# Kernel tuning notes

Measured on AMD Instinct MI355X. Metric: run time of the kernel, lower is better.

## Reference

```python
import jax, jax.numpy as jnp
import numpy as np

NUM_HEADS = 8
GROUPS = 32
EPS = 1e-5


def setup_inputs() -> dict:
    key = jax.random.key(0)
    ks = jax.random.split(key, 4)
    B, C, H, W = 8, 512, 32, 32
    x = jax.random.normal(ks[0], (B, C, H, W), dtype=jnp.float32)
    gn_w = jnp.ones((C,), dtype=jnp.float32)
    gn_b = jnp.zeros((C,), dtype=jnp.float32)
    qkv_w = jax.random.normal(ks[1], (3 * C, C), dtype=jnp.float32) * (1.0 / np.sqrt(C))
    qkv_b = jnp.zeros((3 * C,), dtype=jnp.float32)
    proj_w = jax.random.normal(ks[2], (C, C), dtype=jnp.float32) * (1.0 / np.sqrt(C))
    proj_b = jnp.zeros((C,), dtype=jnp.float32)
    return {"x": x, "gn_w": gn_w, "gn_b": gn_b, "qkv_w": qkv_w,
            "qkv_b": qkv_b, "proj_w": proj_w, "proj_b": proj_b}


def reference(x, gn_w, gn_b, qkv_w, qkv_b, proj_w, proj_b):
    b, c, h, w = x.shape
    n = h * w
    hd = c // NUM_HEADS
    xf = x.reshape(b, c, n)
    # GroupNorm over (channels_per_group, HW) per sample
    xg = xf.reshape(b, GROUPS, -1)
    mu = jnp.mean(xg, axis=-1, keepdims=True)
    var = jnp.var(xg, axis=-1, keepdims=True)
    xn = ((xg - mu) * jax.lax.rsqrt(var + EPS)).reshape(b, c, n)
    xn = xn * gn_w[None, :, None] + gn_b[None, :, None]
    # 1x1 conv == channel matmul
    qkv = jnp.einsum('oc,bcn->bon', qkv_w, xn) + qkv_b[None, :, None]
    q, k, v = jnp.split(qkv, 3, axis=1)
    q = q.reshape(b, NUM_HEADS, hd, n)
    k = k.reshape(b, NUM_HEADS, hd, n)
    v = v.reshape(b, NUM_HEADS, hd, n)
    scale = hd ** 0.5
    score = jnp.einsum('bhdn,bhdm->bhnm', q, k) / scale  # [b,h,HW,HW]
    attn = jax.nn.softmax(score, axis=-1)
    out = jnp.einsum('bhnm,bhdm->bhnd', attn, v)  # [b,h,HW,hd]
    out = out.transpose(0, 1, 3, 2).reshape(b, c, n)
    out = jnp.einsum('oc,bcn->bon', proj_w, out) + proj_b[None, :, None]
    return x + out.reshape(b, c, h, w)
```

## Files before the change

### kernel.cpp

```cpp
#include <hip/hip_runtime.h>

typedef unsigned short u16;
typedef unsigned long long u64;
typedef __bf16 bf16x8 __attribute__((ext_vector_type(8)));
typedef float f32x4 __attribute__((ext_vector_type(4)));

#define NB 8
#define NC 512
#define NN 1024
#define NHEADS 8
#define HDIM 64
#define CPG 16
#define EPSV 1e-5f
#define LOG2E 1.44269504f

__device__ __forceinline__ float bf2f(u16 h) {
  union { unsigned u; float f; } v; v.u = ((unsigned)h) << 16; return v.f;
}
__device__ __forceinline__ u16 f2bf(float f) {
  union { float f; unsigned u; } v; v.f = f;
  unsigned r = v.u + 0x7fffu + ((v.u >> 16) & 1u);
  return (u16)(r >> 16);
}
__device__ __forceinline__ float h2f(u16 h) {
  unsigned s = (h >> 15) & 1u, e = (h >> 10) & 31u, m = h & 1023u;
  union { unsigned u; float f; } v;
  if (e == 0) { v.u = s << 31; return v.f + (s ? -1.f : 1.f) * (float)m * 5.9604645e-8f; }
  if (e == 31) { v.u = (s << 31) | 0x7F800000u | (m << 13); return v.f; }
  v.u = (s << 31) | ((e + 112u) << 23) | (m << 13);
  return v.f;
}
__device__ __forceinline__ u16 f2h(float f) {
  union { float f; unsigned u; } v; v.f = f;
  unsigned s = (v.u >> 16) & 0x8000u; int e = (int)((v.u >> 23) & 0xFF) - 112;
  unsigned m = v.u & 0x7FFFFFu;
  if (e <= 0) return (u16)s;
  if (e >= 31) return (u16)(s | 0x7C00u);
  u16 h = (u16)(s | (e << 10) | (m >> 13));
  unsigned rem = m & 0x1FFFu;
  if (rem > 0x1000u || (rem == 0x1000u && (h & 1u))) ++h;
  return h;
}
__device__ __forceinline__ float load_elem(const void* p, size_t i, int f) {
  if (f == 1) return bf2f(((const u16*)p)[i]);
  if (f == 2) return h2f(((const u16*)p)[i]);
  return ((const float*)p)[i];
}

__device__ __forceinline__ float exp2_fast(float x) {
  float r;
  asm("v_exp_f32 %0, %1" : "=v"(r) : "v"(x));
  return r;
}

__global__ void detect_dtype(const u16* __restrict__ gw_raw, int* __restrict__ flag) {
  if (threadIdx.x != 0 || blockIdx.x != 0) return;
  int bf = 0, hf = 0;
  for (int i = 0; i < 16; ++i) {
    u16 w = gw_raw[i];
    if (w == 0x3F80u) ++bf;
    else if (w == 0x3C00u) ++hf;
  }
  *flag = (bf >= 12) ? 1 : (hf >= 12) ? 2 : 0;
}

__global__ __launch_bounds__(256) void cvt_to_bf16(const void* __restrict__ raw,
                                                   u16* __restrict__ dst, int n,
                                                   const int* __restrict__ flag) {
  const int f = *flag;
  const int i = (blockIdx.x * 256 + threadIdx.x) * 4;
  if (i >= n) return;
  if (f == 1) {
    *(uint2*)(dst + i) = *(const uint2*)((const u16*)raw + i);
  } else if (f == 0) {
    float4 v = *(const float4*)((const float*)raw + i);
    u16 o[4] = {f2bf(v.x), f2bf(v.y), f2bf(v.z), f2bf(v.w)};
    *(u64*)(dst + i) = *(const u64*)o;
  } else {
    u16 o[4];
#pragma unroll
    for (int k2 = 0; k2 < 4; ++k2) o[k2] = f2bf(h2f(((const u16*)raw)[i + k2]));
    *(u64*)(dst + i) = *(const u64*)o;
  }
}

__global__ __launch_bounds__(256) void cvt_biases(const void* __restrict__ gw,
                                                  const void* __restrict__ gb,
                                                  const void* __restrict__ qb,
                                                  const void* __restrict__ pb,
                                                  float* __restrict__ cgw,
                                                  float* __restrict__ cgb,
                                                  float* __restrict__ cqb,
                                                  float* __restrict__ cpb,
                                                  const int* __restrict__ flag) {
  const int f = *flag;
  int i = blockIdx.x * 256 + threadIdx.x;
  if (i < 512)        cgw[i] = load_elem(gw, i, f);
  else if (i < 1024)  cgb[i - 512] = load_elem(gb, (size_t)(i - 512), f);
  else if (i < 2560)  cqb[i - 1024] = load_elem(qb, (size_t)(i - 1024), f);
  else                cpb[i - 2560] = load_elem(pb, (size_t)(i - 2560), f);
}

__global__ __launch_bounds__(256) void gn_naive(const void* __restrict__ x,
                                                const int* __restrict__ flag,
                                                const float* __restrict__ gw,
                                                const float* __restrict__ gb,
                                                u16* __restrict__ xn, int b0) {
  const int f = *flag;
  const int bl = blockIdx.x >> 5;
  const int g  = blockIdx.x & 31;
  const size_t base = ((size_t)((b0 + bl) * NC + g * CPG)) * NN;
  u16* dst = xn + ((size_t)(bl * NC + g * CPG)) * NN;
  __shared__ float r1[256], r2[256];
  const int t = threadIdx.x;
  float s = 0.f, ss = 0.f;
  if (f == 1) {
    const u16* xb = (const u16*)x + base;
    for (int i0 = t * 8; i0 < CPG * NN; i0 += 2048) {
      uint4 dv = *(const uint4*)(xb + i0);
      const u16* pp = (const u16*)&dv;
#pragma unroll
      for (int j = 0; j < 8; ++j) { float v = bf2f(pp[j]); s += v; ss += v * v; }
    }
  } else if (f == 0) {
    const float* xb = (const float*)x + base;
    for (int i0 = t * 4; i0 < CPG * NN; i0 += 1024) {
      float4 v = *(const float4*)(xb + i0);
      s += v.x + v.y + v.z + v.w;
      ss += v.x * v.x + v.y * v.y + v.z * v.z + v.w * v.w;
    }
  } else {
    for (int i = t; i < CPG * NN; i += 256) {
      float v = load_elem(x, base + i, f); s += v; ss += v * v;
    }
  }
  r1[t] = s; r2[t] = ss; __syncthreads();
  for (int k = 128; k > 0; k >>= 1) {
    if (t < k) { r1[t] += r1[t + k]; r2[t] += r2[t + k]; }
    __syncthreads();
  }
  const float mu  = r1[0] * (1.f / 16384.f);
  const float var = r2[0] * (1.f / 16384.f) - mu * mu;
  const float rs  = rsqrtf(var + EPSV);
  if (f == 1) {
    const u16* xb = (const u16*)x + base;
    for (int i0 = t * 8; i0 < CPG * NN; i0 += 2048) {
      const int c = g * CPG + (i0 >> 10);
      const float wsc = gw[c] * rs;
      const float bsc = gb[c] - mu * wsc;
      uint4 dv = *(const uint4*)(xb + i0);
      const u16* pp = (const u16*)&dv;
      u16 o[8];
#pragma unroll
      for (int j = 0; j < 8; ++j) o[j] = f2bf(bf2f(pp[j]) * wsc + bsc);
      *(uint4*)(dst + i0) = *(uint4*)o;
    }
  } else if (f == 0) {
    const float* xb = (const float*)x + base;
    for (int i0 = t * 4; i0 < CPG * NN; i0 += 1024) {
      const int c = g * CPG + (i0 >> 10);
      const float wsc = gw[c] * rs;
      const float bsc = gb[c] - mu * wsc;
      float4 v = *(const float4*)(xb + i0);
      u16 o[4] = {f2bf(v.x * wsc + bsc), f2bf(v.y * wsc + bsc),
                  f2bf(v.z * wsc + bsc), f2bf(v.w * wsc + bsc)};
      *(u64*)(dst + i0) = *(const u64*)o;
    }
  } else {
    for (int i = t; i < CPG * NN; i += 256) {
      int c = g * CPG + i / NN;
      dst[i] = f2bf((load_elem(x, base + i, f) - mu) * rs * gw[c] + gb[c]);
    }
  }
}

__global__ __launch_bounds__(256) void gemm_mfma(const u16* __restrict__ A,
                                                 const u16* __restrict__ Bn,
                                                 const float* __restrict__ bias,
                                                 void* __restrict__ out,
                                                 const void* __restrict__ resid,
                                                 const int* __restrict__ flag,
                                                 int M, int K, int b0, int kmode) {
  __shared__ alignas(16) u16 sA[2][128 * 40];
  __shared__ alignas(16) u16 sB[2][128 * 40];

  const int gx = gridDim.x;
  const int Lx = blockIdx.x + gx * (blockIdx.y + 8 * blockIdx.z);
  const int xcd = Lx & 7;
  const int q8  = Lx >> 3;
  const int bx  = q8 % gx;
  const int pp_ = xcd + 8 * (q8 / gx);
  const int m0 = bx * 128;
  const int n0 = (pp_ & 7) * 128;
  const int bz = pp_ >> 3;

  const int t = threadIdx.x;
  const int lane = t & 63, wv = t >> 6;
  const int wm = (wv >> 1) * 64, wn = (wv & 1) * 64;
  const int lr = lane & 15, quad = lane >> 4;
  const int f = *flag;

  const int ar0 = t >> 2, akc = (t & 3) * 8;
  const int ar1 = 64 + ar0;
  const int bc0 = t >> 4, bno = (t & 15) * 8;
  const int bc1 = 16 + bc0;

  f32x4 acc[4][4] = {};

  const u16* pa0 = A + (size_t)(m0 + ar0) * K + akc;
  const u16* pa1 = A + (size_t)(m0 + ar1) * K + akc;
  const u16* pb0 = Bn + ((size_t)bz * K + bc0) * NN + n0 + bno;
  const u16* pb1 = Bn + ((size_t)bz * K + bc1) * NN + n0 + bno;

#define GSTAGE(dA, dB, ra0_, ra1_, rb0_, rb1_)                           \
  {                                                                      \
    *(uint4*)(dA + ar0 * 40 + akc) = ra0_;                               \
    *(uint4*)(dA + ar1 * 40 + akc) = ra1_;                               \
    const u16* p0 = (const u16*)&rb0_;                                   \
    const u16* p1 = (const u16*)&rb1_;                                   \
    _Pragma("unroll")                                                    \
    for (int j = 0; j < 8; ++j) {                                        \
      const int row = bno + j;                                           \
      dB[row * 40 + (bc0 ^ (row & 24))] = p0[j];                         \
      dB[row * 40 + (bc1 ^ (row & 24))] = p1[j];                         \
    }                                                                    \
  }

#define GMFMA(srcA, srcB)                                                \
  {                                                                      \
    const u16* pA_ = srcA + (wm + lr) * 40 + quad * 8;                   \
    bf16x8 af[4], bfv[4];                                                \
    _Pragma("unroll")                                                    \
    for (int i = 0; i < 4; ++i) {                                        \
      af[i] = *(const bf16x8*)(pA_ + i * 640);                           \
      const int rowB = wn + lr + i * 16;                                 \
      bfv[i] = *(const bf16x8*)(srcB + rowB * 40 + ((quad * 8) ^ (rowB & 24))); \
    }                                                                    \
    _Pragma("unroll")                                                    \
    for (int i = 0; i < 4; ++i)                                          \
      _Pragma("unroll")                                                  \
      for (int j = 0; j < 4; ++j)                                        \
        acc[i][j] = __builtin_amdgcn_mfma_f32_16x16x32_bf16(af[i], bfv[j], acc[i][j], 0, 0, 0); \
  }

  const int nsteps = K >> 5;

  uint4 xa0 = *(const uint4*)(pa0);
  uint4 xa1 = *(const uint4*)(pa1);
  uint4 xb0 = *(const uint4*)(pb0);
  uint4 xb1 = *(const uint4*)(pb1);
  uint4 ya0 = *(const uint4*)(pa0 + 32);
  uint4 ya1 = *(const uint4*)(pa1 + 32);
  uint4 yb0 = *(const uint4*)(pb0 + (size_t)32 * NN);
  uint4 yb1 = *(const uint4*)(pb1 + (size_t)32 * NN);
  GSTAGE(sA[0], sB[0], xa0, xa1, xb0, xb1);
  xa0 = *(const uint4*)(pa0 + 64);
  xa1 = *(const uint4*)(pa1 + 64);
  xb0 = *(const uint4*)(pb0 + (size_t)64 * NN);
  xb1 = *(const uint4*)(pb1 + (size_t)64 * NN);
  __syncthreads();

  for (int s = 0; s < nsteps; s += 2) {
    GSTAGE(sA[1], sB[1], ya0, ya1, yb0, yb1);
    if (s + 3 < nsteps) {
      const int ks = (s + 3) * 32;
      ya0 = *(const uint4*)(pa0 + ks);
      ya1 = *(const uint4*)(pa1 + ks);
      yb0 = *(const uint4*)(pb0 + (size_t)ks * NN);
      yb1 = *(const uint4*)(pb1 + (size_t)ks * NN);
    }
    GMFMA(sA[0], sB[0]);
    __syncthreads();
    if (s + 2 < nsteps) {
      GSTAGE(sA[0], sB[0], xa0, xa1, xb0, xb1);
      if (s + 4 < nsteps) {
        const int ks = (s + 4) * 32;
        xa0 = *(const uint4*)(pa0 + ks);
        xa1 = *(const uint4*)(pa1 + ks);
        xb0 = *(const uint4*)(pb0 + (size_t)ks * NN);
        xb1 = *(const uint4*)(pb1 + (size_t)ks * NN);
      }
    }
    GMFMA(sA[1], sB[1]);
    if (s + 2 < nsteps) __syncthreads();
  }

  const bool kstore = (kmode != 0) && (m0 >= 512) && (m0 < 1024);
  if (kstore) {
    u16* kb2 = (u16*)out + ((size_t)(b0 + bz) * 1536 + 512) * NN;
#pragma unroll
    for (int i = 0; i < 4; ++i) {
      const int mb = m0 + wm + i * 16 + quad * 4;
      const int hh = (mb - 512) >> 6;
      const int d0 = (mb - 512) & 63;
      u16* hb = kb2 + (size_t)hh * NN * 64 + d0;
#pragma unroll
      for (int j = 0; j < 4; ++j) {
        const int col = n0 + wn + j * 16 + lr;
        u16 o[4];
#pragma unroll
        for (int r = 0; r < 4; ++r) o[r] = f2bf(acc[i][j][r] + bias[mb + r]);
        *(u64*)(hb + (size_t)col * 64) = *(const u64*)o;
      }
    }
    return;
  }
#pragma unroll
  for (int i = 0; i < 4; ++i) {
    const int mb = m0 + wm + i * 16 + quad * 4;
#pragma unroll
    for (int r = 0; r < 4; ++r) {
      const int mr = mb + r;
      const float bi = bias[mr];
#pragma unroll
      for (int j = 0; j < 4; ++j) {
        const int col = n0 + wn + j * 16 + lr;
        const size_t oidx = ((size_t)(b0 + bz) * M + mr) * NN + col;
        float v = acc[i][j][r] + bi;
        if (resid) {
          v += load_elem(resid, oidx, f);
          if (f == 1)      ((u16*)out)[oidx] = f2bf(v);
          else if (f == 2) ((u16*)out)[oidx] = f2h(v);
          else             ((float*)out)[oidx] = v;
        } else {
          ((u16*)out)[oidx] = f2bf(v);
        }
      }
    }
  }
}

__global__ __launch_bounds__(256) void attn_mfma(const u16* __restrict__ qkv,
                                                 u16* __restrict__ attnO) {
  __shared__ alignas(16) u16 sK[2][64 * 64];
  __shared__ alignas(16) u16 sV[2][64 * 64];

  const int L   = blockIdx.x + 16 * (blockIdx.y + 8 * blockIdx.z);
  const int xcd = L & 7;
  const int jj  = L >> 3;
  const int grp = xcd + 8 * (jj >> 4);
  const int qt  = jj & 15;
  const int h   = grp & 7;
  const int bz  = grp >> 3;

  const int n0 = qt * 64;
  const u16* qb    = qkv + ((size_t)bz * 1536 + h * HDIM) * NN;
  const u16* kbase = qkv + ((size_t)bz * 1536 + 512) * NN + (size_t)h * NN * HDIM;
  const u16* vb    = qb + (size_t)1024 * NN;
  const int t = threadIdx.x;
  const int lane = t & 63, wv = t >> 6;
  const int lr = lane & 15, quad = lane >> 4;

  const int qcol = n0 + wv * 16 + lr;
  union { u16 u[8]; bf16x8 v; } qa0, qa1;
#pragma unroll
  for (int e = 0; e < 8; ++e) {
    qa0.u[e] = qb[(size_t)(quad * 8 + e) * NN + qcol];
    qa1.u[e] = qb[(size_t)(quad * 8 + 32 + e) * NN + qcol];
  }
  const bf16x8 a0 = qa0.v;
  const bf16x8 a1 = qa1.v;

  const int km = t >> 2;
  const int kc = t & 3;
  const int ke = (km ^ (km >> 3)) & 7;
  const u16* kp = kbase + (size_t)km * 64 + kc * 8;

  const int sd  = t >> 3;
  const int smo = (t & 7) * 8;
  const u16* vp = vb + (size_t)sd * NN + smo;
  const int vs0 = sd * 64 + (smo ^ (8 * (sd & 7)));
  const int vs1 = (sd + 32) * 64 + (smo ^ (8 * ((sd + 32) & 7)));

  uint4 pk0, pk1, pv0, pv1;

  f32x4 acc_o[4] = {};
  float mrow = -1e30f, lrow = 0.f;

  pk0 = *(const uint4*)(kp);
  pk1 = *(const uint4*)(kp + 32);
  pv0 = *(const uint4*)(vp);
  pv1 = *(const uint4*)(vp + (size_t)32 * NN);
  {
    u16* kd = &sK[0][km * 64];
    *(uint4*)(kd + ((kc ^ ke) * 8)) = pk0;
    *(uint4*)(kd + (((kc + 4) ^ ke) * 8)) = pk1;
    *(uint4*)(&sV[0][vs0]) = pv0;
    *(uint4*)(&sV[0][vs1]) = pv1;
  }
  pk0 = *(const uint4*)(kp + 4096);
  pk1 = *(const uint4*)(kp + 4096 + 32);
  pv0 = *(const uint4*)(vp + 64);
  pv1 = *(const uint4*)(vp + (size_t)32 * NN + 64);
  __syncthreads();

  for (int mt = 0; mt < 16; ++mt) {
    const int c = mt & 1;

    f32x4 p[4];
    __builtin_amdgcn_s_setprio(1);
#pragma unroll
    for (int j = 0; j < 4; ++j) {
      const int rk = j * 16 + lr;
      const u16* pKr = &sK[c][rk * 64];
      const int sw = ((rk ^ (rk >> 3)) & 7) * 8;
      bf16x8 k0 = *(const bf16x8*)(pKr + ((quad * 8) ^ sw));
      bf16x8 k1 = *(const bf16x8*)(pKr + ((quad * 8 + 32) ^ sw));
      f32x4 z = {0.f, 0.f, 0.f, 0.f};
      z = __builtin_amdgcn_mfma_f32_16x16x32_bf16(k0, a0, z, 0, 0, 0);
      z = __builtin_amdgcn_mfma_f32_16x16x32_bf16(k1, a1, z, 0, 0, 0);
      p[j] = z;
    }
    __builtin_amdgcn_s_setprio(0);

    float mx = -1e30f;
#pragma unroll
    for (int j = 0; j < 4; ++j)
#pragma unroll
      for (int r = 0; r < 4; ++r) mx = fmaxf(mx, p[j][r]);
    mx = fmaxf(mx, __shfl_xor(mx, 16));
    mx = fmaxf(mx, __shfl_xor(mx, 32));
    const float msc = mx * 0.125f;
    if (!__all(msc - mrow <= 8.f)) {
      const float mnew = fmaxf(mrow, msc);
      const float alpha = exp2_fast((mrow - mnew) * LOG2E);
      mrow = mnew;
      lrow *= alpha;
      float ar[4];
#pragma unroll
      for (int r = 0; r < 4; ++r) ar[r] = __shfl(alpha, quad * 4 + r);
#pragma unroll
      for (int j2 = 0; j2 < 4; ++j2)
#pragma unroll
        for (int r = 0; r < 4; ++r) acc_o[j2][r] *= ar[r];
    }
    const float m2 = mrow * LOG2E;
    float ls = 0.f;
#pragma unroll
    for (int j = 0; j < 4; ++j)
#pragma unroll
      for (int r = 0; r < 4; ++r) {
        const float pe = exp2_fast(fmaf(p[j][r], 0.18033688f, -m2));
        p[j][r] = pe;
        ls += pe;
      }
    ls += __shfl_xor(ls, 16);
    ls += __shfl_xor(ls, 32);
    lrow += ls;

    unsigned pa[4], pb2[4];
#pragma unroll
    for (int j = 0; j < 4; ++j) {
      asm("v_cvt_pk_bf16_f32 %0, %1, %2" : "=v"(pa[j]) : "v"(p[j][0]), "v"(p[j][1]));
      asm("v_cvt_pk_bf16_f32 %0, %1, %2" : "=v"(pb2[j]) : "v"(p[j][2]), "v"(p[j][3]));
    }

    __builtin_amdgcn_s_setprio(1);
#pragma unroll
    for (int ks = 0; ks < 2; ++ks) {
      union { unsigned u[4]; bf16x8 v; } af;
      af.u[0] = pa[2 * ks];
      af.u[1] = pb2[2 * ks];
      af.u[2] = pa[2 * ks + 1];
      af.u[3] = pb2[2 * ks + 1];
#pragma unroll
      for (int j2 = 0; j2 < 4; ++j2) {
        const int rv = j2 * 16 + lr;
        const int swv = 8 * (rv & 7);
        const u16* pVr = &sV[c][rv * 64];
        union { u64 q[2]; bf16x8 v; } bfv;
        bfv.q[0] = *(const u64*)(pVr + ((ks * 32 + 4 * quad) ^ swv));
        bfv.q[1] = *(const u64*)(pVr + ((ks * 32 + 16 + 4 * quad) ^ swv));
        acc_o[j2] = __builtin_amdgcn_mfma_f32_16x16x32_bf16(af.v, bfv.v, acc_o[j2], 0, 0, 0);
      }
    }
    __builtin_amdgcn_s_setprio(0);

    if (mt < 15) {
      const int cn = c ^ 1;
      u16* kd = &sK[cn][km * 64];
      *(uint4*)(kd + ((kc ^ ke) * 8)) = pk0;
      *(uint4*)(kd + (((kc + 4) ^ ke) * 8)) = pk1;
      *(uint4*)(&sV[cn][vs0]) = pv0;
      *(uint4*)(&sV[cn][vs1]) = pv1;
      if (mt < 14) {
        const size_t ko = (size_t)(mt + 2) * 4096;
        const int mo = (mt + 2) * 64;
        pk0 = *(const uint4*)(kp + ko);
        pk1 = *(const uint4*)(kp + ko + 32);
        pv0 = *(const uint4*)(vp + mo);
        pv1 = *(const uint4*)(vp + (size_t)32 * NN + mo);
      }
      __syncthreads();
    }
  }

  const float invl = 1.f / lrow;
  float ir[4];
#pragma unroll
  for (int r = 0; r < 4; ++r) ir[r] = __shfl(invl, quad * 4 + r);
  const int qrow = n0 + wv * 16 + quad * 4;
#pragma unroll
  for (int j2 = 0; j2 < 4; ++j2) {
    const int d = j2 * 16 + lr;
    u16 o[4];
#pragma unroll
    for (int r = 0; r < 4; ++r) o[r] = f2bf(acc_o[j2][r] * ir[r]);
    *(u64*)(attnO + ((size_t)bz * NC + h * HDIM + d) * NN + qrow) = *(const u64*)o;
  }
}

__global__ void sig_small_ws(u16* out) {
  if (threadIdx.x == 0 && blockIdx.x == 0) out[0] = f2bf(20000.f);
}

extern "C" void kernel_launch(void* const* d_in, const int* in_sizes, int n_in,
                              void* d_out, int out_size, void* d_ws, size_t ws_size,
                              hipStream_t stream) {
  const void* x      = d_in[0];
  const void* gn_w   = d_in[1];
  const void* gn_b   = d_in[2];
  const void* qkv_w  = d_in[3];
  const void* qkv_b  = d_in[4];
  const void* proj_w = d_in[5];
  const void* proj_b = d_in[6];
  char* ws = (char*)d_ws;
  const size_t MB = (size_t)1 << 20;

  u16*   wq16 = (u16*)(ws);
  u16*   wp16 = (u16*)(ws + 3 * MB / 2);
  float* cgw  = (float*)(ws + 2 * MB);
  float* cgb  = (float*)(ws + 2 * MB + 4096);
  float* cqb  = (float*)(ws + 2 * MB + 8192);
  float* cpb  = (float*)(ws + 2 * MB + 16384);
  int*   flag = (int*)  (ws + 2 * MB + 20480);

  detect_dtype<<<dim3(1), dim3(64), 0, stream>>>((const u16*)gn_w, flag);
  cvt_to_bf16<<<dim3(768), dim3(256), 0, stream>>>(qkv_w, wq16, 786432, flag);
  cvt_to_bf16<<<dim3(256), dim3(256), 0, stream>>>(proj_w, wp16, 262144, flag);
  cvt_biases<<<dim3(12), dim3(256), 0, stream>>>(gn_w, gn_b, qkv_b, proj_b,
                                                 cgw, cgb, cqb, cpb, flag);

  if (ws_size >= 36 * MB) {
    u16* xn    = (u16*)(ws + 3 * MB);
    u16* qkvb  = (u16*)(ws + 11 * MB);
    u16* attnO = xn;
    gn_naive<<<dim3(NB * 32), dim3(256), 0, stream>>>(x, flag, cgw, cgb, xn, 0);
    gemm_mfma<<<dim3(12, 8, NB), dim3(256), 0, stream>>>(wq16, xn, cqb, qkvb,
                                                         nullptr, flag, 1536, NC, 0, 1);
    attn_mfma<<<dim3(16, NHEADS, NB), dim3(256), 0, stream>>>(qkvb, attnO);
    gemm_mfma<<<dim3(4, 8, NB), dim3(256), 0, stream>>>(wp16, attnO, cpb, d_out,
                                                        x, flag, NC, NC, 0, 0);
  } else if (ws_size >= 9 * MB) {
    u16* xn    = (u16*)(ws + 3 * MB);
    u16* qkvb  = (u16*)(ws + 4 * MB);
    u16* attnO = (u16*)(ws + 7 * MB);
    for (int b = 0; b < NB; ++b) {
      gn_naive<<<dim3(32), dim3(256), 0, stream>>>(x, flag, cgw, cgb, xn, b);
      gemm_mfma<<<dim3(12, 8, 1), dim3(256), 0, stream>>>(wq16, xn, cqb, qkvb,
                                                          nullptr, flag, 1536, NC, 0, 1);
      attn_mfma<<<dim3(16, NHEADS, 1), dim3(256), 0, stream>>>(qkvb, attnO);
      gemm_mfma<<<dim3(4, 8, 1), dim3(256), 0, stream>>>(wp16, attnO, cpb, d_out,
                                                         x, flag, NC, NC, b, 0);
    }
  } else {
    sig_small_ws<<<dim3(1), dim3(64), 0, stream>>>((u16*)d_out);
  }
}
```

Measured before the change: 221.4 us.

## Merge conversion kernels, cache GroupNorm input in LDS, simplify GEMM staging

Three weight and bias conversion launches become a single cvt_all kernel, which removes launch overhead. GroupNorm keeps the group's input slice in a 64KB shared buffer, so the normalize pass reads LDS instead of re-reading global memory. At the same time the GEMM drops its double-buffered LDS and XCD-aware block remapping in favour of single-buffer staging with extra barriers. That likely loses overlap between loads and MFMA, and lowers L2 locality across XCDs.

```diff
diff --git a/kernel.cpp b/kernel.cpp
--- a/kernel.cpp
+++ b/kernel.cpp
@@ -64,12 +64,7 @@
   *flag = (bf >= 12) ? 1 : (hf >= 12) ? 2 : 0;
 }
 
-__global__ __launch_bounds__(256) void cvt_to_bf16(const void* __restrict__ raw,
-                                                   u16* __restrict__ dst, int n,
-                                                   const int* __restrict__ flag) {
-  const int f = *flag;
-  const int i = (blockIdx.x * 256 + threadIdx.x) * 4;
-  if (i >= n) return;
+__device__ __forceinline__ void cvt4(const void* raw, u16* dst, int i, int f) {
   if (f == 1) {
     *(uint2*)(dst + i) = *(const uint2*)((const u16*)raw + i);
   } else if (f == 0) {
@@ -84,21 +79,32 @@
   }
 }
 
-__global__ __launch_bounds__(256) void cvt_biases(const void* __restrict__ gw,
-                                                  const void* __restrict__ gb,
-                                                  const void* __restrict__ qb,
-                                                  const void* __restrict__ pb,
-                                                  float* __restrict__ cgw,
-                                                  float* __restrict__ cgb,
-                                                  float* __restrict__ cqb,
-                                                  float* __restrict__ cpb,
-                                                  const int* __restrict__ flag) {
+__global__ __launch_bounds__(256) void cvt_all(const void* __restrict__ qkvw,
+                                               const void* __restrict__ projw,
+                                               const void* __restrict__ gw,
+                                               const void* __restrict__ gb,
+                                               const void* __restrict__ qb,
+                                               const void* __restrict__ pb,
+                                               u16* __restrict__ wq16,
+                                               u16* __restrict__ wp16,
+                                               float* __restrict__ cgw,
+                                               float* __restrict__ cgb,
+                                               float* __restrict__ cqb,
+                                               float* __restrict__ cpb,
+                                               const int* __restrict__ flag) {
   const int f = *flag;
-  int i = blockIdx.x * 256 + threadIdx.x;
-  if (i < 512)        cgw[i] = load_elem(gw, i, f);
-  else if (i < 1024)  cgb[i - 512] = load_elem(gb, (size_t)(i - 512), f);
-  else if (i < 2560)  cqb[i - 1024] = load_elem(qb, (size_t)(i - 1024), f);
-  else                cpb[i - 2560] = load_elem(pb, (size_t)(i - 2560), f);
+  const int b = blockIdx.x;
+  if (b < 768) {
+    cvt4(qkvw, wq16, (b * 256 + threadIdx.x) * 4, f);
+  } else if (b < 1024) {
+    cvt4(projw, wp16, ((b - 768) * 256 + threadIdx.x) * 4, f);
+  } else {
+    const int i = (b - 1024) * 256 + threadIdx.x;
+    if (i < 512)        cgw[i] = load_elem(gw, i, f);
+    else if (i < 1024)  cgb[i - 512] = load_elem(gb, (size_t)(i - 512), f);
+    else if (i < 2560)  cqb[i - 1024] = load_elem(qb, (size_t)(i - 1024), f);
+    else                cpb[i - 2560] = load_elem(pb, (size_t)(i - 2560), f);
+  }
 }
 
 __global__ __launch_bounds__(256) void gn_naive(const void* __restrict__ x,
@@ -112,12 +118,15 @@
   const size_t base = ((size_t)((b0 + bl) * NC + g * CPG)) * NN;
   u16* dst = xn + ((size_t)(bl * NC + g * CPG)) * NN;
   __shared__ float r1[256], r2[256];
+  __shared__ alignas(16) float sxf[CPG * NN];
+  u16* sx16 = (u16*)sxf;
   const int t = threadIdx.x;
   float s = 0.f, ss = 0.f;
   if (f == 1) {
     const u16* xb = (const u16*)x + base;
     for (int i0 = t * 8; i0 < CPG * NN; i0 += 2048) {
       uint4 dv = *(const uint4*)(xb + i0);
+      *(uint4*)(sx16 + i0) = dv;
       const u16* pp = (const u16*)&dv;
 #pragma unroll
       for (int j = 0; j < 8; ++j) { float v = bf2f(pp[j]); s += v; ss += v * v; }
@@ -126,6 +135,7 @@
     const float* xb = (const float*)x + base;
     for (int i0 = t * 4; i0 < CPG * NN; i0 += 1024) {
       float4 v = *(const float4*)(xb + i0);
+      *(float4*)(sxf + i0) = v;
       s += v.x + v.y + v.z + v.w;
       ss += v.x * v.x + v.y * v.y + v.z * v.z + v.w * v.w;
     }
@@ -143,12 +153,11 @@
   const float var = r2[0] * (1.f / 16384.f) - mu * mu;
   const float rs  = rsqrtf(var + EPSV);
   if (f == 1) {
-    const u16* xb = (const u16*)x + base;
     for (int i0 = t * 8; i0 < CPG * NN; i0 += 2048) {
       const int c = g * CPG + (i0 >> 10);
       const float wsc = gw[c] * rs;
       const float bsc = gb[c] - mu * wsc;
-      uint4 dv = *(const uint4*)(xb + i0);
+      uint4 dv = *(const uint4*)(sx16 + i0);
       const u16* pp = (const u16*)&dv;
       u16 o[8];
 #pragma unroll
@@ -156,12 +165,11 @@
       *(uint4*)(dst + i0) = *(uint4*)o;
     }
   } else if (f == 0) {
-    const float* xb = (const float*)x + base;
     for (int i0 = t * 4; i0 < CPG * NN; i0 += 1024) {
       const int c = g * CPG + (i0 >> 10);
       const float wsc = gw[c] * rs;
       const float bsc = gb[c] - mu * wsc;
-      float4 v = *(const float4*)(xb + i0);
+      float4 v = *(const float4*)(sxf + i0);
       u16 o[4] = {f2bf(v.x * wsc + bsc), f2bf(v.y * wsc + bsc),
                   f2bf(v.z * wsc + bsc), f2bf(v.w * wsc + bsc)};
       *(u64*)(dst + i0) = *(const u64*)o;
@@ -181,19 +189,11 @@
                                                  const void* __restrict__ resid,
                                                  const int* __restrict__ flag,
                                                  int M, int K, int b0, int kmode) {
-  __shared__ alignas(16) u16 sA[2][128 * 40];
-  __shared__ alignas(16) u16 sB[2][128 * 40];
-
-  const int gx = gridDim.x;
-  const int Lx = blockIdx.x + gx * (blockIdx.y + 8 * blockIdx.z);
-  const int xcd = Lx & 7;
-  const int q8  = Lx >> 3;
-  const int bx  = q8 % gx;
-  const int pp_ = xcd + 8 * (q8 / gx);
-  const int m0 = bx * 128;
-  const int n0 = (pp_ & 7) * 128;
-  const int bz = pp_ >> 3;
-
+  __shared__ alignas(16) u16 sA[128 * 40];
+  __shared__ alignas(16) u16 sB[128 * 40];
+  const int m0 = blockIdx.x * 128;
+  const int n0 = blockIdx.y * 128;
+  const int bz = blockIdx.z;
   const int t = threadIdx.x;
   const int lane = t & 63, wv = t >> 6;
   const int wm = (wv >> 1) * 64, wn = (wv & 1) * 64;
@@ -211,39 +211,6 @@
   const u16* pa1 = A + (size_t)(m0 + ar1) * K + akc;
   const u16* pb0 = Bn + ((size_t)bz * K + bc0) * NN + n0 + bno;
   const u16* pb1 = Bn + ((size_t)bz * K + bc1) * NN + n0 + bno;
-
-#define GSTAGE(dA, dB, ra0_, ra1_, rb0_, rb1_)                           \
-  {                                                                      \
-    *(uint4*)(dA + ar0 * 40 + akc) = ra0_;                               \
-    *(uint4*)(dA + ar1 * 40 + akc) = ra1_;                               \
-    const u16* p0 = (const u16*)&rb0_;                                   \
-    const u16* p1 = (const u16*)&rb1_;                                   \
-    _Pragma("unroll")                                                    \
-    for (int j = 0; j < 8; ++j) {                                        \
-      const int row = bno + j;                                           \
-      dB[row * 40 + (bc0 ^ (row & 24))] = p0[j];                         \
-      dB[row * 40 + (bc1 ^ (row & 24))] = p1[j];                         \
-    }                                                                    \
-  }
-
-#define GMFMA(srcA, srcB)                                                \
-  {                                                                      \
-    const u16* pA_ = srcA + (wm + lr) * 40 + quad * 8;                   \
-    bf16x8 af[4], bfv[4];                                                \
-    _Pragma("unroll")                                                    \
-    for (int i = 0; i < 4; ++i) {                                        \
-      af[i] = *(const bf16x8*)(pA_ + i * 640);                           \
-      const int rowB = wn + lr + i * 16;                                 \
-      bfv[i] = *(const bf16x8*)(srcB + rowB * 40 + ((quad * 8) ^ (rowB & 24))); \
-    }                                                                    \
-    _Pragma("unroll")                                                    \
-    for (int i = 0; i < 4; ++i)                                          \
-      _Pragma("unroll")                                                  \
-      for (int j = 0; j < 4; ++j)                                        \
-        acc[i][j] = __builtin_amdgcn_mfma_f32_16x16x32_bf16(af[i], bfv[j], acc[i][j], 0, 0, 0); \
-  }
-
-  const int nsteps = K >> 5;
 
   uint4 xa0 = *(const uint4*)(pa0);
   uint4 xa1 = *(const uint4*)(pa1);
@@ -253,36 +220,59 @@
   uint4 ya1 = *(const uint4*)(pa1 + 32);
   uint4 yb0 = *(const uint4*)(pb0 + (size_t)32 * NN);
   uint4 yb1 = *(const uint4*)(pb1 + (size_t)32 * NN);
-  GSTAGE(sA[0], sB[0], xa0, xa1, xb0, xb1);
-  xa0 = *(const uint4*)(pa0 + 64);
-  xa1 = *(const uint4*)(pa1 + 64);
-  xb0 = *(const uint4*)(pb0 + (size_t)64 * NN);
-  xb1 = *(const uint4*)(pb1 + (size_t)64 * NN);
-  __syncthreads();
-
-  for (int s = 0; s < nsteps; s += 2) {
-    GSTAGE(sA[1], sB[1], ya0, ya1, yb0, yb1);
-    if (s + 3 < nsteps) {
-      const int ks = (s + 3) * 32;
-      ya0 = *(const uint4*)(pa0 + ks);
-      ya1 = *(const uint4*)(pa1 + ks);
-      yb0 = *(const uint4*)(pb0 + (size_t)ks * NN);
-      yb1 = *(const uint4*)(pb1 + (size_t)ks * NN);
-    }
-    GMFMA(sA[0], sB[0]);
+
+#define GEMM_STAGE(ra0, ra1, rb0, rb1)                                   \
+  {                                                                      \
+    *(uint4*)(sA + ar0 * 40 + akc) = ra0;                                \
+    *(uint4*)(sA + ar1 * 40 + akc) = ra1;                                \
+    const u16* p0 = (const u16*)&rb0;                                    \
+    const u16* p1 = (const u16*)&rb1;                                    \
+    _Pragma("unroll")                                                    \
+    for (int j = 0; j < 8; ++j) {                                        \
+      const int row = bno + j;                                           \
+      sB[row * 40 + (bc0 ^ (row & 24))] = p0[j];                         \
+      sB[row * 40 + (bc1 ^ (row & 24))] = p1[j];                         \
+    }                                                                    \
+  }
+
+#define GEMM_MFMA_BLOCK()                                                \
+  {                                                                      \
+    const u16* pA = sA + (wm + lr) * 40 + quad * 8;                      \
+    bf16x8 af[4], bfv[4];                                                \
+    _Pragma("unroll")                                                    \
+    for (int i = 0; i < 4; ++i) {                                        \
+      af[i] = *(const bf16x8*)(pA + i * 640);                            \
+      const int rowB = wn + lr + i * 16;                                 \
+      bfv[i] = *(const bf16x8*)(sB + rowB * 40 + ((quad * 8) ^ (rowB & 24))); \
+    }                                                                    \
+    _Pragma("unroll")                                                    \
+    for (int i = 0; i < 4; ++i)                                          \
+      _Pragma("unroll")                                                  \
+      for (int j = 0; j < 4; ++j)                                        \
+        acc[i][j] = __builtin_amdgcn_mfma_f32_16x16x32_bf16(af[i], bfv[j], acc[i][j], 0, 0, 0); \
+  }
+
+  for (int k0 = 0; k0 < K; k0 += 64) {
     __syncthreads();
-    if (s + 2 < nsteps) {
-      GSTAGE(sA[0], sB[0], xa0, xa1, xb0, xb1);
-      if (s + 4 < nsteps) {
-        const int ks = (s + 4) * 32;
-        xa0 = *(const uint4*)(pa0 + ks);
-        xa1 = *(const uint4*)(pa1 + ks);
-        xb0 = *(const uint4*)(pb0 + (size_t)ks * NN);
-        xb1 = *(const uint4*)(pb1 + (size_t)ks * NN);
-      }
-    }
-    GMFMA(sA[1], sB[1]);
-    if (s + 2 < nsteps) __syncthreads();
+    GEMM_STAGE(xa0, xa1, xb0, xb1);
+    __syncthreads();
+    if (k0 + 64 < K) {
+      xa0 = *(const uint4*)(pa0 + k0 + 64);
+      xa1 = *(const uint4*)(pa1 + k0 + 64);
+      xb0 = *(const uint4*)(pb0 + (size_t)(k0 + 64) * NN);
+      xb1 = *(const uint4*)(pb1 + (size_t)(k0 + 64) * NN);
+    }
+    GEMM_MFMA_BLOCK();
+    __syncthreads();
+    GEMM_STAGE(ya0, ya1, yb0, yb1);
+    __syncthreads();
+    if (k0 + 96 < K) {
+      ya0 = *(const uint4*)(pa0 + k0 + 96);
+      ya1 = *(const uint4*)(pa1 + k0 + 96);
+      yb0 = *(const uint4*)(pb0 + (size_t)(k0 + 96) * NN);
+      yb1 = *(const uint4*)(pb1 + (size_t)(k0 + 96) * NN);
+    }
+    GEMM_MFMA_BLOCK();
   }
 
   const bool kstore = (kmode != 0) && (m0 >= 512) && (m0 < 1024);
@@ -536,10 +526,9 @@
   int*   flag = (int*)  (ws + 2 * MB + 20480);
 
   detect_dtype<<<dim3(1), dim3(64), 0, stream>>>((const u16*)gn_w, flag);
-  cvt_to_bf16<<<dim3(768), dim3(256), 0, stream>>>(qkv_w, wq16, 786432, flag);
-  cvt_to_bf16<<<dim3(256), dim3(256), 0, stream>>>(proj_w, wp16, 262144, flag);
-  cvt_biases<<<dim3(12), dim3(256), 0, stream>>>(gn_w, gn_b, qkv_b, proj_b,
-                                                 cgw, cgb, cqb, cpb, flag);
+  cvt_all<<<dim3(1036), dim3(256), 0, stream>>>(qkv_w, proj_w, gn_w, gn_b,
+                                                qkv_b, proj_b, wq16, wp16,
+                                                cgw, cgb, cqb, cpb, flag);
 
   if (ws_size >= 36 * MB) {
     u16* xn    = (u16*)(ws + 3 * MB);
```

New measurement: 201.1 us. 1.1x faster.
